# Kernel optimization log

Hardware: AMD Instinct MI355X
Metric: run time of the kernel (lower is better)

## Reference

```python
import jax, jax.numpy as jnp
import numpy as np

B, P, K, HE, HF = 256, 128, 512, 1024, 512
D = K + HE + 2 * HF  # 2560, MLP input dim
HID = 64


def setup_inputs() -> dict:
    key = jax.random.key(0)
    ks = jax.random.split(key, 6)
    query = jax.random.normal(ks[0], (B, 1, HE), dtype=jnp.float32)
    keys = jax.random.normal(ks[1], (B, P, K), dtype=jnp.float32)
    frameLSTM_h = jax.random.normal(ks[2], (B, 1, 2 * HF), dtype=jnp.float32)
    mask = jax.random.randint(ks[3], (B, P), 0, 2, dtype=jnp.int32)
    mask = mask.at[:, 0].set(1)  # guarantee at least one unmasked player per row
    W1 = jax.random.normal(ks[4], (D, HID), dtype=jnp.float32) / np.float32(np.sqrt(D))
    W2 = jax.random.normal(ks[5], (HID, 1), dtype=jnp.float32) / np.float32(np.sqrt(HID))
    return dict(query=query, keys=keys, frameLSTM_h=frameLSTM_h, mask=mask, W1=W1, W2=W2)


def reference(query, keys, frameLSTM_h, mask, W1, W2):
    # Faithful to: cat([keys, query.repeat, frame.repeat]) @ W1 -> ReLU -> @ W2.
    # The pre-activation is linear, so splitting W1 by row-blocks is exactly the
    # same math without materializing the repeated/concatenated (B,P,D) tensor.
    W1k = W1[:K]            # (K, 64)
    W1q = W1[K:K + HE]      # (HE, 64)
    W1f = W1[K + HE:]       # (2*HF, 64)
    h = jax.nn.relu(
        jnp.einsum('bpk,kh->bph', keys, W1k)
        + jnp.einsum('boe,eh->boh', query, W1q)        # broadcasts over P
        + jnp.einsum('bof,fh->boh', frameLSTM_h, W1f)  # broadcasts over P
    )  # (B, P, 64)
    raw_scores = jnp.einsum('bph,ho->bp', h, W2)  # (B, P)
    raw_scores = jnp.where(mask == 0, -jnp.inf, raw_scores)
    weights = jax.nn.softmax(raw_scores, axis=1)  # (B, P)
    context = jnp.einsum('bp,bpk->bk', weights, keys)[:, None, :]  # (B, 1, K)
    embeddings = jnp.concatenate([context, frameLSTM_h], axis=2)   # (B, 1, K+2*HF)
    return embeddings, weights
```

## Files before the change

### kernel.cpp

```cpp
#include <hip/hip_runtime.h>
#include <hip/hip_bf16.h>
#include <cstdint>
#include <math.h>


typedef __bf16 bf16;
typedef __attribute__((ext_vector_type(8))) __bf16 bf16x8;
typedef __attribute__((ext_vector_type(4))) __bf16 bf16x4;
typedef __attribute__((ext_vector_type(4))) float f32x4;

#define NB 256
#define NP 128
#define NK 512
#define SKLD 520
#define SK_BYTES (NP * SKLD * 2)
#define SMEM_BYTES (SK_BYTES + 128*4 + 128*4 + 64*4 + 64*4)

__global__ __launch_bounds__(256) void prep_kernel(
    const float* __restrict__ query, const float* __restrict__ frame,
    const float* __restrict__ W1, bf16* __restrict__ w1kt,
    float* __restrict__ proj_part)
{
    const int blk = blockIdx.x;
    const int t = threadIdx.x;
    if (blk < 512) {
        __shared__ float part[4][64];
        const int b = blk >> 1;
        const int half = blk & 1;
        const int h = t & 63;
        const int g = t >> 6;
        const float* src = (half == 0 ? query : frame) + (size_t)b * 1024 + g * 256;
        const float* wrow = W1 + (size_t)(512 + half * 1024 + g * 256) * 64 + h;
        float acc = 0.f;
#pragma unroll 8
        for (int dd = 0; dd < 256; dd++)
            acc += src[dd] * wrow[(size_t)dd * 64];
        part[g][h] = acc;
        __syncthreads();
        if (t < 64)
            proj_part[((size_t)half * NB + b) * 64 + t] =
                part[0][t] + part[1][t] + part[2][t] + part[3][t];
    } else {
        __shared__ float s[32][65];
        const int j = blk - 512;
        const int k0 = j * 32;
#pragma unroll
        for (int i = 0; i < 8; i++) {
            const int idx = t + 256 * i;
            const int k = idx >> 6, h = idx & 63;
            s[k][h] = W1[(size_t)(k0 + k) * 64 + h];
        }
        __syncthreads();
#pragma unroll
        for (int i = 0; i < 8; i++) {
            const int idx = t + 256 * i;
            const int h = idx >> 5, kk = idx & 31;
            w1kt[(size_t)h * 512 + k0 + kk] = (bf16)s[kk][h];
        }
    }
}

__global__ __launch_bounds__(256) void attn_kernel(
    const float* __restrict__ keys, const float* __restrict__ frame,
    const int* __restrict__ mask, const float* __restrict__ W2,
    const bf16* __restrict__ w1kt, const float* __restrict__ proj_part,
    float* __restrict__ out)
{
    extern __shared__ char smem[];
    bf16* sk       = (bf16*)smem;
    float* scores  = (float*)(smem + SK_BYTES);
    float* wts     = scores + 128;
    float* projl   = wts + 128;
    float* w2l     = projl + 64;

    const int b = blockIdx.x;
    const int t = threadIdx.x;

    if (t < 64) projl[t] = proj_part[(size_t)b * 64 + t]
                         + proj_part[((size_t)NB + b) * 64 + t];
    else if (t < 128) w2l[t - 64] = W2[t - 64];

    const float* kb = keys + (size_t)b * (NP * NK);
    {
        const int rowadd = (t >> 7);
        const int c0 = (t & 127) * 4;
#pragma unroll 8
        for (int i = 0; i < 64; i++) {
            const float4 v = *(const float4*)(kb + (size_t)i * 1024 + t * 4);
            bf16x4 bv;
            bv[0] = (bf16)v.x; bv[1] = (bf16)v.y; bv[2] = (bf16)v.z; bv[3] = (bf16)v.w;
            *(bf16x4*)(sk + (2 * i + rowadd) * SKLD + c0) = bv;
        }
    }
    __syncthreads();

    const int w = t >> 6;
    const int lane = t & 63;
    const int m = lane & 15;
    const int q = lane >> 4;
    const int pw = w * 32;

    f32x4 acc[2][4];
#pragma unroll
    for (int a = 0; a < 2; a++)
#pragma unroll
        for (int n = 0; n < 4; n++) acc[a][n] = (f32x4){0.f, 0.f, 0.f, 0.f};

    for (int kk = 0; kk < 16; kk++) {
        const int k0 = kk * 32 + q * 8;
        const bf16x8 A0 = *(const bf16x8*)(sk + (pw + m) * SKLD + k0);
        const bf16x8 A1 = *(const bf16x8*)(sk + (pw + 16 + m) * SKLD + k0);
#pragma unroll
        for (int nt = 0; nt < 4; nt++) {
            const bf16x8 Bf = *(const bf16x8*)(w1kt + (size_t)(nt * 16 + m) * 512 + k0);
            acc[0][nt] = __builtin_amdgcn_mfma_f32_16x16x32_bf16(A0, Bf, acc[0][nt], 0, 0, 0);
            acc[1][nt] = __builtin_amdgcn_mfma_f32_16x16x32_bf16(A1, Bf, acc[1][nt], 0, 0, 0);
        }
    }

#pragma unroll
    for (int mt = 0; mt < 2; mt++) {
        float p0 = 0.f, p1 = 0.f, p2 = 0.f, p3 = 0.f;
#pragma unroll
        for (int nt = 0; nt < 4; nt++) {
            const int h = nt * 16 + m;
            const float pr = projl[h];
            const float w2v = w2l[h];
            const f32x4 c = acc[mt][nt];
            p0 += fmaxf(c[0] + pr, 0.f) * w2v;
            p1 += fmaxf(c[1] + pr, 0.f) * w2v;
            p2 += fmaxf(c[2] + pr, 0.f) * w2v;
            p3 += fmaxf(c[3] + pr, 0.f) * w2v;
        }
#pragma unroll
        for (int off = 1; off < 16; off <<= 1) {
            p0 += __shfl_xor(p0, off);
            p1 += __shfl_xor(p1, off);
            p2 += __shfl_xor(p2, off);
            p3 += __shfl_xor(p3, off);
        }
        if (m == 0) {
            const int pbase = pw + mt * 16 + q * 4;
            scores[pbase + 0] = p0; scores[pbase + 1] = p1;
            scores[pbase + 2] = p2; scores[pbase + 3] = p3;
        }
    }
    __syncthreads();

    if (w == 0) {
        const int pa = lane, pb = lane + 64;
        float s0 = (mask[b * 128 + pa] == 0) ? -INFINITY : scores[pa];
        float s1 = (mask[b * 128 + pb] == 0) ? -INFINITY : scores[pb];
        float mx = fmaxf(s0, s1);
#pragma unroll
        for (int off = 32; off; off >>= 1) mx = fmaxf(mx, __shfl_xor(mx, off));
        float e0 = __expf(s0 - mx), e1 = __expf(s1 - mx);
        float sum = e0 + e1;
#pragma unroll
        for (int off = 32; off; off >>= 1) sum += __shfl_xor(sum, off);
        const float inv = 1.0f / sum;
        e0 *= inv; e1 *= inv;
        wts[pa] = e0; wts[pb] = e1;
        float* wout = out + (size_t)NB * 1536;
        wout[b * 128 + pa] = e0;
        wout[b * 128 + pb] = e1;
    }
    __syncthreads();

    {
        float a0 = 0.f, a1 = 0.f;
        const int c = 2 * t;
#pragma unroll 8
        for (int p = 0; p < 128; p++) {
            const float wv = wts[p];
            const uint32_t uv = *(const uint32_t*)(sk + p * SKLD + c);
            const float f0 = __uint_as_float(uv << 16);
            const float f1 = __uint_as_float(uv & 0xffff0000u);
            a0 += wv * f0;
            a1 += wv * f1;
        }
        out[(size_t)b * 1536 + c] = a0;
        out[(size_t)b * 1536 + c + 1] = a1;
    }
    {
        const float4 fv = *(const float4*)(frame + (size_t)b * 1024 + t * 4);
        *(float4*)(out + (size_t)b * 1536 + 512 + t * 4) = fv;
    }
}

extern "C" void kernel_launch(void* const* d_in, const int* in_sizes, int n_in,
                              void* d_out, int out_size, void* d_ws, size_t ws_size,
                              hipStream_t stream) {
    const float* query = (const float*)d_in[0];
    const float* keys  = (const float*)d_in[1];
    const float* frame = (const float*)d_in[2];
    const int*   mask  = (const int*)d_in[3];
    const float* W1    = (const float*)d_in[4];
    const float* W2    = (const float*)d_in[5];
    float* out = (float*)d_out;

    bf16*  w1kt      = (bf16*)d_ws;
    float* proj_part = (float*)((char*)d_ws + 65536);

    hipFuncSetAttribute((const void*)attn_kernel,
                        hipFuncAttributeMaxDynamicSharedMemorySize, SMEM_BYTES);

    prep_kernel<<<528, 256, 0, stream>>>(query, frame, W1, w1kt, proj_part);
    attn_kernel<<<256, 256, SMEM_BYTES, stream>>>(keys, frame, mask, W2, w1kt, proj_part, out);
}
```

Baseline: 126.5 us.

## Split attention into score and context kernels with more blocks per batch

Splits the fused attention kernel in two. The first kernel computes scores on half a batch row per block (512 blocks, 2 per CU) and prefetches the W1 fragments in registers. The second kernel does the masked softmax and re-reads keys from global memory in fp32 to form the context. The prep kernel also splits the query/frame projection into quarters for more parallelism. The aim is better occupancy and more blocks in flight, at the cost of reading keys twice and an extra launch. Context is now computed from fp32 keys rather than bf16.

```diff
diff --git a/kernel.cpp b/kernel.cpp
--- a/kernel.cpp
+++ b/kernel.cpp
@@ -13,8 +13,8 @@
 #define NP 128
 #define NK 512
 #define SKLD 520
-#define SK_BYTES (NP * SKLD * 2)
-#define SMEM_BYTES (SK_BYTES + 128*4 + 128*4 + 64*4 + 64*4)
+#define K1_SK_BYTES (64 * SKLD * 2)
+#define K1_SMEM (K1_SK_BYTES + 64*4 + 64*4)
 
 __global__ __launch_bounds__(256) void prep_kernel(
     const float* __restrict__ query, const float* __restrict__ frame,
@@ -23,26 +23,26 @@
 {
     const int blk = blockIdx.x;
     const int t = threadIdx.x;
-    if (blk < 512) {
+    if (blk < 1024) {
         __shared__ float part[4][64];
-        const int b = blk >> 1;
-        const int half = blk & 1;
+        const int b = blk >> 2;
+        const int q4 = blk & 3;
         const int h = t & 63;
         const int g = t >> 6;
-        const float* src = (half == 0 ? query : frame) + (size_t)b * 1024 + g * 256;
-        const float* wrow = W1 + (size_t)(512 + half * 1024 + g * 256) * 64 + h;
+        const float* src = (q4 < 2 ? query : frame) + (size_t)b * 1024 + (q4 & 1) * 512 + g * 128;
+        const float* wrow = W1 + (size_t)(512 + q4 * 512 + g * 128) * 64 + h;
         float acc = 0.f;
 #pragma unroll 8
-        for (int dd = 0; dd < 256; dd++)
+        for (int dd = 0; dd < 128; dd++)
             acc += src[dd] * wrow[(size_t)dd * 64];
         part[g][h] = acc;
         __syncthreads();
         if (t < 64)
-            proj_part[((size_t)half * NB + b) * 64 + t] =
+            proj_part[((size_t)q4 * NB + b) * 64 + t] =
                 part[0][t] + part[1][t] + part[2][t] + part[3][t];
     } else {
         __shared__ float s[32][65];
-        const int j = blk - 512;
+        const int j = blk - 1024;
         const int k0 = j * 32;
 #pragma unroll
         for (int i = 0; i < 8; i++) {
@@ -60,32 +60,33 @@
     }
 }
 
-__global__ __launch_bounds__(256) void attn_kernel(
-    const float* __restrict__ keys, const float* __restrict__ frame,
-    const int* __restrict__ mask, const float* __restrict__ W2,
+__global__ __launch_bounds__(256, 2) void k1_scores(
+    const float* __restrict__ keys, const float* __restrict__ W2,
     const bf16* __restrict__ w1kt, const float* __restrict__ proj_part,
-    float* __restrict__ out)
+    float* __restrict__ scores_ws)
 {
     extern __shared__ char smem[];
-    bf16* sk       = (bf16*)smem;
-    float* scores  = (float*)(smem + SK_BYTES);
-    float* wts     = scores + 128;
-    float* projl   = wts + 128;
-    float* w2l     = projl + 64;
-
-    const int b = blockIdx.x;
+    bf16* sk     = (bf16*)smem;
+    float* projl = (float*)(smem + K1_SK_BYTES);
+    float* w2l   = projl + 64;
+
+    const int b    = blockIdx.x >> 1;
+    const int half = blockIdx.x & 1;
     const int t = threadIdx.x;
 
-    if (t < 64) projl[t] = proj_part[(size_t)b * 64 + t]
-                         + proj_part[((size_t)NB + b) * 64 + t];
+    if (t < 64)
+        projl[t] = proj_part[(size_t)b * 64 + t]
+                 + proj_part[((size_t)NB + b) * 64 + t]
+                 + proj_part[((size_t)2 * NB + b) * 64 + t]
+                 + proj_part[((size_t)3 * NB + b) * 64 + t];
     else if (t < 128) w2l[t - 64] = W2[t - 64];
 
-    const float* kb = keys + (size_t)b * (NP * NK);
+    const float* kb = keys + (size_t)b * (NP * NK) + (size_t)half * 64 * NK;
     {
         const int rowadd = (t >> 7);
         const int c0 = (t & 127) * 4;
 #pragma unroll 8
-        for (int i = 0; i < 64; i++) {
+        for (int i = 0; i < 32; i++) {
             const float4 v = *(const float4*)(kb + (size_t)i * 1024 + t * 4);
             bf16x4 bv;
             bv[0] = (bf16)v.x; bv[1] = (bf16)v.y; bv[2] = (bf16)v.z; bv[3] = (bf16)v.w;
@@ -98,59 +99,78 @@
     const int lane = t & 63;
     const int m = lane & 15;
     const int q = lane >> 4;
-    const int pw = w * 32;
-
-    f32x4 acc[2][4];
-#pragma unroll
-    for (int a = 0; a < 2; a++)
-#pragma unroll
-        for (int n = 0; n < 4; n++) acc[a][n] = (f32x4){0.f, 0.f, 0.f, 0.f};
-
+
+    const bf16* bbase = w1kt + (size_t)m * 512 + q * 8;
+    bf16x8 Bc[4], Bn[4];
+#pragma unroll
+    for (int nt = 0; nt < 4; nt++) Bc[nt] = *(const bf16x8*)(bbase + nt * 8192);
+#pragma unroll
+    for (int nt = 0; nt < 4; nt++) Bn[nt] = *(const bf16x8*)(bbase + nt * 8192 + 32);
+
+    f32x4 acc[4];
+#pragma unroll
+    for (int nt = 0; nt < 4; nt++) acc[nt] = (f32x4){0.f, 0.f, 0.f, 0.f};
+
+#pragma unroll
     for (int kk = 0; kk < 16; kk++) {
-        const int k0 = kk * 32 + q * 8;
-        const bf16x8 A0 = *(const bf16x8*)(sk + (pw + m) * SKLD + k0);
-        const bf16x8 A1 = *(const bf16x8*)(sk + (pw + 16 + m) * SKLD + k0);
-#pragma unroll
-        for (int nt = 0; nt < 4; nt++) {
-            const bf16x8 Bf = *(const bf16x8*)(w1kt + (size_t)(nt * 16 + m) * 512 + k0);
-            acc[0][nt] = __builtin_amdgcn_mfma_f32_16x16x32_bf16(A0, Bf, acc[0][nt], 0, 0, 0);
-            acc[1][nt] = __builtin_amdgcn_mfma_f32_16x16x32_bf16(A1, Bf, acc[1][nt], 0, 0, 0);
-        }
-    }
-
-#pragma unroll
-    for (int mt = 0; mt < 2; mt++) {
-        float p0 = 0.f, p1 = 0.f, p2 = 0.f, p3 = 0.f;
-#pragma unroll
-        for (int nt = 0; nt < 4; nt++) {
-            const int h = nt * 16 + m;
-            const float pr = projl[h];
-            const float w2v = w2l[h];
-            const f32x4 c = acc[mt][nt];
-            p0 += fmaxf(c[0] + pr, 0.f) * w2v;
-            p1 += fmaxf(c[1] + pr, 0.f) * w2v;
-            p2 += fmaxf(c[2] + pr, 0.f) * w2v;
-            p3 += fmaxf(c[3] + pr, 0.f) * w2v;
-        }
-#pragma unroll
-        for (int off = 1; off < 16; off <<= 1) {
-            p0 += __shfl_xor(p0, off);
-            p1 += __shfl_xor(p1, off);
-            p2 += __shfl_xor(p2, off);
-            p3 += __shfl_xor(p3, off);
-        }
-        if (m == 0) {
-            const int pbase = pw + mt * 16 + q * 4;
-            scores[pbase + 0] = p0; scores[pbase + 1] = p1;
-            scores[pbase + 2] = p2; scores[pbase + 3] = p3;
-        }
-    }
-    __syncthreads();
-
-    if (w == 0) {
-        const int pa = lane, pb = lane + 64;
-        float s0 = (mask[b * 128 + pa] == 0) ? -INFINITY : scores[pa];
-        float s1 = (mask[b * 128 + pb] == 0) ? -INFINITY : scores[pb];
+        const bf16x8 A = *(const bf16x8*)(sk + (w * 16 + m) * SKLD + kk * 32 + q * 8);
+        bf16x8 Bf[4];
+#pragma unroll
+        for (int nt = 0; nt < 4; nt++) Bf[nt] = Bc[nt];
+#pragma unroll
+        for (int nt = 0; nt < 4; nt++) Bc[nt] = Bn[nt];
+        if (kk < 14) {
+#pragma unroll
+            for (int nt = 0; nt < 4; nt++)
+                Bn[nt] = *(const bf16x8*)(bbase + nt * 8192 + (kk + 2) * 32);
+        }
+#pragma unroll
+        for (int nt = 0; nt < 4; nt++)
+            acc[nt] = __builtin_amdgcn_mfma_f32_16x16x32_bf16(A, Bf[nt], acc[nt], 0, 0, 0);
+    }
+
+    float pr[4] = {0.f, 0.f, 0.f, 0.f};
+#pragma unroll
+    for (int nt = 0; nt < 4; nt++) {
+        const int h = nt * 16 + m;
+        const float pv = projl[h];
+        const float wv = w2l[h];
+#pragma unroll
+        for (int r = 0; r < 4; r++)
+            pr[r] += fmaxf(acc[nt][r] + pv, 0.f) * wv;
+    }
+#pragma unroll
+    for (int off = 1; off < 16; off <<= 1) {
+#pragma unroll
+        for (int r = 0; r < 4; r++) pr[r] += __shfl_xor(pr[r], off);
+    }
+    if (m == 0) {
+        const int base = b * 128 + half * 64 + w * 16 + q * 4;
+#pragma unroll
+        for (int r = 0; r < 4; r++) scores_ws[base + r] = pr[r];
+    }
+}
+
+__global__ __launch_bounds__(512) void k2_context(
+    const float* __restrict__ keys, const float* __restrict__ frame,
+    const int* __restrict__ mask, const float* __restrict__ scores_ws,
+    float* __restrict__ out)
+{
+    __shared__ float s_sc[128];
+    __shared__ float s_w[128];
+    __shared__ float part[512];
+
+    const int b = blockIdx.x;
+    const int t = threadIdx.x;
+
+    if (t < 128) {
+        const float raw = scores_ws[b * 128 + t];
+        s_sc[t] = (mask[b * 128 + t] == 0) ? -INFINITY : raw;
+    }
+    __syncthreads();
+
+    if (t < 64) {
+        float s0 = s_sc[t], s1 = s_sc[t + 64];
         float mx = fmaxf(s0, s1);
 #pragma unroll
         for (int off = 32; off; off >>= 1) mx = fmaxf(mx, __shfl_xor(mx, off));
@@ -159,33 +179,37 @@
 #pragma unroll
         for (int off = 32; off; off >>= 1) sum += __shfl_xor(sum, off);
         const float inv = 1.0f / sum;
-        e0 *= inv; e1 *= inv;
-        wts[pa] = e0; wts[pb] = e1;
-        float* wout = out + (size_t)NB * 1536;
-        wout[b * 128 + pa] = e0;
-        wout[b * 128 + pb] = e1;
-    }
-    __syncthreads();
-
-    {
-        float a0 = 0.f, a1 = 0.f;
-        const int c = 2 * t;
+        s_w[t] = e0 * inv;
+        s_w[t + 64] = e1 * inv;
+    }
+    __syncthreads();
+
+    if (t < 128) out[(size_t)NB * 1536 + b * 128 + t] = s_w[t];
+
+    const int tg = t >> 8;
+    const int tc = t & 255;
+    const float* kb = keys + (size_t)b * (NP * NK);
+    float a0 = 0.f, a1 = 0.f;
 #pragma unroll 8
-        for (int p = 0; p < 128; p++) {
-            const float wv = wts[p];
-            const uint32_t uv = *(const uint32_t*)(sk + p * SKLD + c);
-            const float f0 = __uint_as_float(uv << 16);
-            const float f1 = __uint_as_float(uv & 0xffff0000u);
-            a0 += wv * f0;
-            a1 += wv * f1;
-        }
-        out[(size_t)b * 1536 + c] = a0;
-        out[(size_t)b * 1536 + c + 1] = a1;
-    }
-    {
-        const float4 fv = *(const float4*)(frame + (size_t)b * 1024 + t * 4);
-        *(float4*)(out + (size_t)b * 1536 + 512 + t * 4) = fv;
-    }
+    for (int i = 0; i < 64; i++) {
+        const int p = tg * 64 + i;
+        const float wv = s_w[p];
+        const float2 v = *(const float2*)(kb + (size_t)p * 512 + 2 * tc);
+        a0 += wv * v.x;
+        a1 += wv * v.y;
+    }
+    if (tg == 1) {
+        part[2 * tc] = a0;
+        part[2 * tc + 1] = a1;
+    }
+    __syncthreads();
+    if (tg == 0) {
+        out[(size_t)b * 1536 + 2 * tc]     = a0 + part[2 * tc];
+        out[(size_t)b * 1536 + 2 * tc + 1] = a1 + part[2 * tc + 1];
+    }
+
+    out[(size_t)b * 1536 + 512 + t] = frame[(size_t)b * 1024 + t];
+    out[(size_t)b * 1536 + 1024 + t] = frame[(size_t)b * 1024 + 512 + t];
 }
 
 extern "C" void kernel_launch(void* const* d_in, const int* in_sizes, int n_in,
@@ -200,11 +224,13 @@
     float* out = (float*)d_out;
 
     bf16*  w1kt      = (bf16*)d_ws;
-    float* proj_part = (float*)((char*)d_ws + 65536);
-
-    hipFuncSetAttribute((const void*)attn_kernel,
-                        hipFuncAttributeMaxDynamicSharedMemorySize, SMEM_BYTES);
-
-    prep_kernel<<<528, 256, 0, stream>>>(query, frame, W1, w1kt, proj_part);
-    attn_kernel<<<256, 256, SMEM_BYTES, stream>>>(keys, frame, mask, W2, w1kt, proj_part, out);
-}
+    float* proj_part = (float*)((char*)d_ws + (64 << 10));
+    float* scores_ws = (float*)((char*)d_ws + (320 << 10));
+
+    hipFuncSetAttribute((const void*)k1_scores,
+                        hipFuncAttributeMaxDynamicSharedMemorySize, K1_SMEM);
+
+    prep_kernel<<<1040, 256, 0, stream>>>(query, frame, W1, w1kt, proj_part);
+    k1_scores<<<512, 256, K1_SMEM, stream>>>(keys, W2, w1kt, proj_part, scores_ws);
+    k2_context<<<256, 512, 0, stream>>>(keys, frame, mask, scores_ws, out);
+}
```

Result: slower. 138.3 us (+9.3%).

## Double-buffer key loads, prefetch W1 fragments in registers, split projection across more blocks

Applied to the files above, without the earlier changes.

The keys staging loop now issues 16 float4 loads per batch into a register double buffer, so global loads for the next batch overlap the bf16 conversion and LDS stores of the current one. The MFMA loop is reordered to go over output tiles first, with all 16 B-fragments per tile prefetched into registers one tile ahead and the ReLU/W2 epilogue applied per tile. The prep kernel splits the query/frame projection into four quarters per batch (1024 blocks), giving more parallelism and shorter serial loops, and the attention kernel sums four partials. The cost is much higher register pressure (two 16-entry float4 buffers and two 16-entry bf16x8 buffers), which may reduce occupancy or cause spills.

```diff
diff --git a/kernel.cpp b/kernel.cpp
--- a/kernel.cpp
+++ b/kernel.cpp
@@ -23,26 +23,26 @@
 {
     const int blk = blockIdx.x;
     const int t = threadIdx.x;
-    if (blk < 512) {
+    if (blk < 1024) {
         __shared__ float part[4][64];
-        const int b = blk >> 1;
-        const int half = blk & 1;
+        const int b = blk >> 2;
+        const int q4 = blk & 3;
         const int h = t & 63;
         const int g = t >> 6;
-        const float* src = (half == 0 ? query : frame) + (size_t)b * 1024 + g * 256;
-        const float* wrow = W1 + (size_t)(512 + half * 1024 + g * 256) * 64 + h;
+        const float* src = (q4 < 2 ? query : frame) + (size_t)b * 1024 + (q4 & 1) * 512 + g * 128;
+        const float* wrow = W1 + (size_t)(512 + q4 * 512 + g * 128) * 64 + h;
         float acc = 0.f;
 #pragma unroll 8
-        for (int dd = 0; dd < 256; dd++)
+        for (int dd = 0; dd < 128; dd++)
             acc += src[dd] * wrow[(size_t)dd * 64];
         part[g][h] = acc;
         __syncthreads();
         if (t < 64)
-            proj_part[((size_t)half * NB + b) * 64 + t] =
+            proj_part[((size_t)q4 * NB + b) * 64 + t] =
                 part[0][t] + part[1][t] + part[2][t] + part[3][t];
     } else {
         __shared__ float s[32][65];
-        const int j = blk - 512;
+        const int j = blk - 1024;
         const int k0 = j * 32;
 #pragma unroll
         for (int i = 0; i < 8; i++) {
@@ -67,29 +67,47 @@
     float* __restrict__ out)
 {
     extern __shared__ char smem[];
-    bf16* sk       = (bf16*)smem;
-    float* scores  = (float*)(smem + SK_BYTES);
-    float* wts     = scores + 128;
-    float* projl   = wts + 128;
-    float* w2l     = projl + 64;
+    bf16* sk      = (bf16*)smem;
+    float* scores = (float*)(smem + SK_BYTES);
+    float* wts    = scores + 128;
+    float* projl  = wts + 128;
+    float* w2l    = projl + 64;
 
     const int b = blockIdx.x;
     const int t = threadIdx.x;
 
-    if (t < 64) projl[t] = proj_part[(size_t)b * 64 + t]
-                         + proj_part[((size_t)NB + b) * 64 + t];
+    if (t < 64)
+        projl[t] = proj_part[(size_t)b * 64 + t]
+                 + proj_part[((size_t)NB + b) * 64 + t]
+                 + proj_part[((size_t)2 * NB + b) * 64 + t]
+                 + proj_part[((size_t)3 * NB + b) * 64 + t];
     else if (t < 128) w2l[t - 64] = W2[t - 64];
 
     const float* kb = keys + (size_t)b * (NP * NK);
     {
-        const int rowadd = (t >> 7);
+        const int rowadd = t >> 7;
         const int c0 = (t & 127) * 4;
-#pragma unroll 8
-        for (int i = 0; i < 64; i++) {
-            const float4 v = *(const float4*)(kb + (size_t)i * 1024 + t * 4);
-            bf16x4 bv;
-            bv[0] = (bf16)v.x; bv[1] = (bf16)v.y; bv[2] = (bf16)v.z; bv[3] = (bf16)v.w;
-            *(bf16x4*)(sk + (2 * i + rowadd) * SKLD + c0) = bv;
+        float4 kv[2][16];
+#pragma unroll
+        for (int ii = 0; ii < 16; ii++)
+            kv[0][ii] = *(const float4*)(kb + (size_t)ii * 1024 + t * 4);
+#pragma unroll
+        for (int jj = 0; jj < 4; jj++) {
+            const int cur = jj & 1;
+            if (jj < 3) {
+#pragma unroll
+                for (int ii = 0; ii < 16; ii++)
+                    kv[cur ^ 1][ii] =
+                        *(const float4*)(kb + (size_t)((jj + 1) * 16 + ii) * 1024 + t * 4);
+            }
+#pragma unroll
+            for (int ii = 0; ii < 16; ii++) {
+                const float4 v = kv[cur][ii];
+                bf16x4 bv;
+                bv[0] = (bf16)v.x; bv[1] = (bf16)v.y;
+                bv[2] = (bf16)v.z; bv[3] = (bf16)v.w;
+                *(bf16x4*)(sk + (size_t)(2 * (jj * 16 + ii) + rowadd) * SKLD + c0) = bv;
+            }
         }
     }
     __syncthreads();
@@ -100,49 +118,57 @@
     const int q = lane >> 4;
     const int pw = w * 32;
 
-    f32x4 acc[2][4];
-#pragma unroll
-    for (int a = 0; a < 2; a++)
-#pragma unroll
-        for (int n = 0; n < 4; n++) acc[a][n] = (f32x4){0.f, 0.f, 0.f, 0.f};
-
-    for (int kk = 0; kk < 16; kk++) {
-        const int k0 = kk * 32 + q * 8;
-        const bf16x8 A0 = *(const bf16x8*)(sk + (pw + m) * SKLD + k0);
-        const bf16x8 A1 = *(const bf16x8*)(sk + (pw + 16 + m) * SKLD + k0);
-#pragma unroll
-        for (int nt = 0; nt < 4; nt++) {
-            const bf16x8 Bf = *(const bf16x8*)(w1kt + (size_t)(nt * 16 + m) * 512 + k0);
-            acc[0][nt] = __builtin_amdgcn_mfma_f32_16x16x32_bf16(A0, Bf, acc[0][nt], 0, 0, 0);
-            acc[1][nt] = __builtin_amdgcn_mfma_f32_16x16x32_bf16(A1, Bf, acc[1][nt], 0, 0, 0);
-        }
-    }
-
-#pragma unroll
-    for (int mt = 0; mt < 2; mt++) {
-        float p0 = 0.f, p1 = 0.f, p2 = 0.f, p3 = 0.f;
-#pragma unroll
-        for (int nt = 0; nt < 4; nt++) {
-            const int h = nt * 16 + m;
-            const float pr = projl[h];
-            const float w2v = w2l[h];
-            const f32x4 c = acc[mt][nt];
-            p0 += fmaxf(c[0] + pr, 0.f) * w2v;
-            p1 += fmaxf(c[1] + pr, 0.f) * w2v;
-            p2 += fmaxf(c[2] + pr, 0.f) * w2v;
-            p3 += fmaxf(c[3] + pr, 0.f) * w2v;
-        }
-#pragma unroll
-        for (int off = 1; off < 16; off <<= 1) {
-            p0 += __shfl_xor(p0, off);
-            p1 += __shfl_xor(p1, off);
-            p2 += __shfl_xor(p2, off);
-            p3 += __shfl_xor(p3, off);
-        }
-        if (m == 0) {
+    const bf16* bbase = w1kt + (size_t)m * 512 + q * 8;
+
+    bf16x8 Bv[2][16];
+#pragma unroll
+    for (int kk = 0; kk < 16; kk++)
+        Bv[0][kk] = *(const bf16x8*)(bbase + kk * 32);
+
+    float pr[2][4] = {{0.f,0.f,0.f,0.f},{0.f,0.f,0.f,0.f}};
+
+#pragma unroll
+    for (int nt = 0; nt < 4; nt++) {
+        const int cur = nt & 1;
+        if (nt < 3) {
+#pragma unroll
+            for (int kk = 0; kk < 16; kk++)
+                Bv[cur ^ 1][kk] = *(const bf16x8*)(bbase + (nt + 1) * 8192 + kk * 32);
+        }
+        f32x4 acc0 = (f32x4){0.f,0.f,0.f,0.f};
+        f32x4 acc1 = (f32x4){0.f,0.f,0.f,0.f};
+#pragma unroll
+        for (int kk = 0; kk < 16; kk++) {
+            const int k0 = kk * 32 + q * 8;
+            const bf16x8 A0 = *(const bf16x8*)(sk + (pw + m) * SKLD + k0);
+            const bf16x8 A1 = *(const bf16x8*)(sk + (pw + 16 + m) * SKLD + k0);
+            acc0 = __builtin_amdgcn_mfma_f32_16x16x32_bf16(A0, Bv[cur][kk], acc0, 0, 0, 0);
+            acc1 = __builtin_amdgcn_mfma_f32_16x16x32_bf16(A1, Bv[cur][kk], acc1, 0, 0, 0);
+        }
+        const int h = nt * 16 + m;
+        const float pv = projl[h];
+        const float wv = w2l[h];
+#pragma unroll
+        for (int r = 0; r < 4; r++) {
+            pr[0][r] += fmaxf(acc0[r] + pv, 0.f) * wv;
+            pr[1][r] += fmaxf(acc1[r] + pv, 0.f) * wv;
+        }
+    }
+
+#pragma unroll
+    for (int off = 1; off < 16; off <<= 1) {
+#pragma unroll
+        for (int mt = 0; mt < 2; mt++)
+#pragma unroll
+            for (int r = 0; r < 4; r++)
+                pr[mt][r] += __shfl_xor(pr[mt][r], off);
+    }
+    if (m == 0) {
+#pragma unroll
+        for (int mt = 0; mt < 2; mt++) {
             const int pbase = pw + mt * 16 + q * 4;
-            scores[pbase + 0] = p0; scores[pbase + 1] = p1;
-            scores[pbase + 2] = p2; scores[pbase + 3] = p3;
+#pragma unroll
+            for (int r = 0; r < 4; r++) scores[pbase + r] = pr[mt][r];
         }
     }
     __syncthreads();
@@ -174,10 +200,8 @@
         for (int p = 0; p < 128; p++) {
             const float wv = wts[p];
             const uint32_t uv = *(const uint32_t*)(sk + p * SKLD + c);
-            const float f0 = __uint_as_float(uv << 16);
-            const float f1 = __uint_as_float(uv & 0xffff0000u);
-            a0 += wv * f0;
-            a1 += wv * f1;
+            a0 += wv * __uint_as_float(uv << 16);
+            a1 += wv * __uint_as_float(uv & 0xffff0000u);
         }
         out[(size_t)b * 1536 + c] = a0;
         out[(size_t)b * 1536 + c + 1] = a1;
@@ -200,11 +224,12 @@
     float* out = (float*)d_out;
 
     bf16*  w1kt      = (bf16*)d_ws;
-    float* proj_part = (float*)((char*)d_ws + 65536);
+    float* proj_part = (float*)((char*)d_ws + (64 << 10));
 
     hipFuncSetAttribute((const void*)attn_kernel,
                         hipFuncAttributeMaxDynamicSharedMemorySize, SMEM_BYTES);
 
-    prep_kernel<<<528, 256, 0, stream>>>(query, frame, W1, w1kt, proj_part);
-    attn_kernel<<<256, 256, SMEM_BYTES, stream>>>(keys, frame, mask, W2, w1kt, proj_part, out);
+    prep_kernel<<<1040, 256, 0, stream>>>(query, frame, W1, w1kt, proj_part);
+    attn_kernel<<<256, 256, SMEM_BYTES, stream>>>(keys, frame, mask, W2, w1kt,
+                                                  proj_part, out);
 }
```

After: 123.5 us. 2.4% less time.
